# Optimization experiments

Hardware: AMD Instinct MI355X
Metric: run time of the kernel (lower is better)

Reference implementation:

```python
import jax, jax.numpy as jnp
import numpy as np

BLK = 128            # weight_block_size for w8a16 blockwise dequant
H = 1024             # hidden_size
I = 512              # moe_intermediate_size
E = 64               # n_routed_experts
T = 512              # tokens (seq_len)
K = 6                # num_experts_per_tok
G = 8                # n_group
TG = 3               # topk_group
NSH = 2              # n_shared_experts
I2 = I * NSH         # shared expert intermediate size
ROUTED_SCALE = 2.5
NORM_TOPK = True


def dq(w_int8, scale, blk=BLK):
    """Blockwise w8a16 dequant: w [..., M, N] int8, scale [..., M/blk, N/blk] f32."""
    *lead, M, N = w_int8.shape
    w = w_int8.astype(scale.dtype).reshape(*lead, M // blk, blk, N // blk, blk)
    return (w * scale[..., :, None, :, None]).reshape(*lead, M, N)


def setup_inputs() -> dict:
    key = jax.random.key(0)
    ks = jax.random.split(key, 16)
    ri = lambda k, shp: jax.random.randint(k, shp, -8, 8, dtype=jnp.int8)
    rs = lambda k, shp: jax.random.uniform(k, shp, minval=0.01, maxval=0.03, dtype=jnp.float32)
    return {
        "x": jax.random.normal(ks[0], (T, H), jnp.float32),
        "gate_w": jax.random.normal(ks[1], (E, H), jnp.float32) * 0.02,  # router gate [E,H]
        "wg": ri(ks[2], (E, I, H)),  "sg": rs(ks[3], (E, I // BLK, H // BLK)),
        "wu": ri(ks[4], (E, I, H)),  "su": rs(ks[5], (E, I // BLK, H // BLK)),
        "wd": ri(ks[6], (E, I, H)),  "sd": rs(ks[7], (E, I // BLK, H // BLK)),  # down, transposed layout [I,H]
        "sh_wg": ri(ks[8], (I2, H)),  "sh_sg": rs(ks[9], (I2 // BLK, H // BLK)),
        "sh_wu": ri(ks[10], (I2, H)), "sh_su": rs(ks[11], (I2 // BLK, H // BLK)),
        "sh_wd": ri(ks[12], (I2, H)), "sh_sd": rs(ks[13], (I2 // BLK, H // BLK)),
    }


def _moe(x, gate_w, wg, sg, wu, su, wd, sd, sh_wg, sh_sg, sh_wu, sh_su, sh_wd, sh_sd):
    Tn = x.shape[0]
    # --- router: sigmoid scoring + group-limited top-k ---
    scores = jax.nn.sigmoid(x @ gate_w.T)                       # [T, E]
    gsz = E // G
    group_scores = scores.reshape(Tn, G, gsz).max(axis=-1)      # [T, G]
    _, gidx = jax.lax.top_k(group_scores, TG)                   # [T, TG]
    gmask = jax.nn.one_hot(gidx, G, dtype=scores.dtype).sum(1)  # [T, G]
    emask = jnp.repeat(gmask, gsz, axis=-1)                     # [T, E]
    masked = jnp.where(emask > 0, scores, -jnp.inf)
    w, idx = jax.lax.top_k(masked, K)                           # [T, K]
    if NORM_TOPK:
        w = w / (w.sum(-1, keepdims=True) + 1e-20)
    w = w * ROUTED_SCALE
    # per-token combine weights over experts
    comb = (jax.nn.one_hot(idx, E, dtype=x.dtype) * w[:, :, None]).sum(1)  # [T, E]

    # --- routed experts: dequantized silu-gated MLPs, masked dense combine ---
    Wg, Wu, Wd = dq(wg, sg), dq(wu, su), dq(wd, sd)             # [E, I, H]
    g = jnp.einsum('th,eih->eti', x, Wg)                        # [E, T, I]
    u = jnp.einsum('th,eih->eti', x, Wu)
    hmid = jax.nn.silu(g) * u
    y = jnp.einsum('eti,eih->eth', hmid, Wd)                    # [E, T, H]
    routed = jnp.einsum('eth,te->th', y, comb)                  # [T, H]

    # --- shared experts MLP ---
    Sg, Su, Sd = dq(sh_wg, sh_sg), dq(sh_wu, sh_su), dq(sh_wd, sh_sd)
    shared = (jax.nn.silu(x @ Sg.T) * (x @ Su.T)) @ Sd          # [T, H]
    return routed + shared


def reference(x, gate_w, wg, sg, wu, su, wd, sd, sh_wg, sh_sg, sh_wu, sh_su, sh_wd, sh_sd):
    return _moe(x, gate_w, wg, sg, wu, su, wd, sd,
                sh_wg, sh_sg, sh_wu, sh_su, sh_wd, sh_sd)
```

## Files before the change

### kernel.cpp

```cpp
#include <hip/hip_runtime.h>
#include <math.h>
#include <stdint.h>

#define T_   512
#define H_   1024
#define I_   512
#define E_   64
#define K_   6
#define G_   8
#define TG_  3
#define EB_  80

typedef _Float16 h8 __attribute__((ext_vector_type(8)));
typedef _Float16 h4v __attribute__((ext_vector_type(4)));
typedef float    f4 __attribute__((ext_vector_type(4)));

__global__ __launch_bounds__(64) void router_k(
    const float* __restrict__ x, const float* __restrict__ gw,
    int* __restrict__ cnt, int* __restrict__ tlist, float* __restrict__ wlist)
{
  const int t   = blockIdx.x;
  const int tid = threadIdx.x;
  __shared__ float sx[H_];
  __shared__ float sc[E_];

  for (int h4 = tid; h4 < H_/4; h4 += 64)
    ((float4*)sx)[h4] = ((const float4*)(x + (size_t)t*H_))[h4];
  __syncthreads();

  const float* wr = gw + (size_t)tid * H_;
  float acc = 0.f;
  for (int h = 0; h < H_; h += 4) {
    float4 xv = *(const float4*)(sx + h);
    float4 wv = *(const float4*)(wr + h);
    acc = fmaf(xv.x, wv.x, acc); acc = fmaf(xv.y, wv.y, acc);
    acc = fmaf(xv.z, wv.z, acc); acc = fmaf(xv.w, wv.w, acc);
  }
  sc[tid] = 1.f / (1.f + expf(-acc));
  __syncthreads();

  if (tid == 0) {
    float gs[G_];
    #pragma unroll
    for (int g = 0; g < G_; g++) {
      float m = sc[g*8];
      #pragma unroll
      for (int j = 1; j < 8; j++) m = fmaxf(m, sc[g*8+j]);
      gs[g] = m;
    }
    unsigned gp = 0;
    for (int r = 0; r < TG_; r++) {
      int best = 0; float bv = -1e30f;
      for (int g = 0; g < G_; g++)
        if (!((gp >> g) & 1) && gs[g] > bv) { bv = gs[g]; best = g; }
      gp |= 1u << best;
    }
    int   eidx[K_]; float ew[K_];
    unsigned long long em = 0ull;
    float wsum = 0.f;
    for (int r = 0; r < K_; r++) {
      int best = 0; float bv = -1e30f;
      for (int e = 0; e < E_; e++) {
        if (!((gp >> (e >> 3)) & 1)) continue;
        if ((em >> e) & 1ull) continue;
        if (sc[e] > bv) { bv = sc[e]; best = e; }
      }
      em |= 1ull << best; eidx[r] = best; ew[r] = bv; wsum += bv;
    }
    const float inv = 2.5f / (wsum + 1e-20f);
    for (int r = 0; r < K_; r++) {
      int e = eidx[r];
      int pos = atomicAdd(&cnt[e], 1);
      tlist[e*T_ + pos] = (t << 13) | (t*K_ + r);
      wlist[e*T_ + pos] = ew[r] * inv;
    }
  }
}

__global__ void pseudo_init_k(int* cnt, int* tlist, float* wlist) {
  int s = blockIdx.x*256 + threadIdx.x;
  if (s == 0) { cnt[64] = T_; cnt[65] = T_; }
  if (s < 1024) {
    int e = 64 + (s >> 9);
    int t = s & 511;
    tlist[e*T_ + t] = (t << 13) | (3072 + s);
    wlist[e*T_ + t] = 1.0f;
  }
}

__global__ __launch_bounds__(256) void xh_prep_k(
    const float* __restrict__ x, _Float16* __restrict__ xh)
{
  int i = blockIdx.x*256 + threadIdx.x;
  float4 v = ((const float4*)x)[i];
  h4v o = { (_Float16)v.x, (_Float16)v.y, (_Float16)v.z, (_Float16)v.w };
  *(h4v*)(xh + (size_t)i*4) = o;
}

__device__ __forceinline__ void eb_decode(int eb, const int* cnt,
                                          int& e, int& lo, int& hi) {
  if (eb < E_) { e = eb; lo = 0; hi = cnt[e]; }
  else { int q = (eb - E_) & 7; e = E_ + ((eb - E_) >> 3); lo = q*64; hi = lo + 64; }
}

__device__ __forceinline__ h8 cvt8i(int4 a, int4 b) {
  union { _Float16 f[8]; h8 v; } t;
  t.f[0]=(_Float16)a.x; t.f[1]=(_Float16)a.y; t.f[2]=(_Float16)a.z; t.f[3]=(_Float16)a.w;
  t.f[4]=(_Float16)b.x; t.f[5]=(_Float16)b.y; t.f[6]=(_Float16)b.z; t.f[7]=(_Float16)b.w;
  return t.v;
}

#define NKT_G 16

#define GU_STEP(KT, WN)                                                       \
  do {                                                                        \
    asm volatile("s_waitcnt vmcnt(" #WN ") lgkmcnt(0)" ::: "memory");         \
    __builtin_amdgcn_sched_barrier(0);                                        \
    __builtin_amdgcn_s_barrier();                                             \
    if ((KT) + 1 < NKT_G)                                                     \
      *(h8*)(wdst + (((KT)+1)&1)*4608) =                                      \
          cvt8i(Wr[((KT)+1)%3][0], Wr[((KT)+1)%3][1]);                        \
    if ((KT) + 3 < NKT_G) {                                                   \
      Wr[((KT)+3)%3][0] = *(const int4*)(wsrc + ((KT)+3)*64);                 \
      Wr[((KT)+3)%3][1] = *(const int4*)(wsrc + ((KT)+3)*64 + 4);             \
    }                                                                         \
    {                                                                         \
      const char* tb = tb0 + (((KT)&1))*4608;                                 \
      h8 bg0 = *(const h8*)(tb);                                              \
      h8 bg1 = *(const h8*)(tb + 64);                                         \
      h8 bu0 = *(const h8*)(tb + 2304);                                       \
      h8 bu1 = *(const h8*)(tb + 2304 + 64);                                  \
      if (((KT)&1) == 0) { partg = (f4){0.f,0.f,0.f,0.f}; partu = partg; }    \
      partg = __builtin_amdgcn_mfma_f32_16x16x32_f16(Ar[(KT)%3][0], bg0, partg, 0,0,0); \
      partg = __builtin_amdgcn_mfma_f32_16x16x32_f16(Ar[(KT)%3][1], bg1, partg, 0,0,0); \
      partu = __builtin_amdgcn_mfma_f32_16x16x32_f16(Ar[(KT)%3][0], bu0, partu, 0,0,0); \
      partu = __builtin_amdgcn_mfma_f32_16x16x32_f16(Ar[(KT)%3][1], bu1, partu, 0,0,0); \
      if (((KT)&1) == 1) {                                                    \
        totg += partg * sgv[(KT)>>1];                                         \
        totu += partu * suv[(KT)>>1];                                         \
      }                                                                       \
    }                                                                         \
    if ((KT) + 3 < NKT_G) {                                                   \
      Ar[((KT)+3)%3][0] = *(const h8*)(ax + ((KT)+3)*64);                     \
      Ar[((KT)+3)%3][1] = *(const h8*)(ax + ((KT)+3)*64 + 32);                \
    }                                                                         \
  } while (0)

__global__ __launch_bounds__(256, 6) void gateup_k(
    const _Float16* __restrict__ xh,
    const int* __restrict__ wg, const float* __restrict__ sg,
    const int* __restrict__ wu, const float* __restrict__ su,
    const int* __restrict__ shwg, const float* __restrict__ shsg,
    const int* __restrict__ shwu, const float* __restrict__ shsu,
    const int* __restrict__ cnt, const int* __restrict__ tlist,
    const float* __restrict__ wlist,
    _Float16* __restrict__ hmid)
{
  const int ic = blockIdx.x;
  const int eb = blockIdx.y;
  int e, lo, hi;
  eb_decode(eb, cnt, e, lo, hi);
  if (hi <= lo) return;

  const int tid  = threadIdx.x;
  const int lane = tid & 63;
  const int wv   = tid >> 6;
  const int mr   = lane & 15;
  const int quad = lane >> 4;

  const int *wgb, *wub; const float *sgp, *sup; int sib;
  if (e < E_) {
    wgb = wg + (size_t)e*I_*H_;  wub = wu + (size_t)e*I_*H_;
    sgp = sg + e*32;  sup = su + e*32;  sib = ic >> 3;
  } else {
    int hf = e - E_;
    wgb = shwg + (size_t)hf*512*H_;  wub = shwu + (size_t)hf*512*H_;
    sgp = shsg;  sup = shsu;  sib = hf*4 + (ic >> 3);
  }
  float sgv[8], suv[8];
  #pragma unroll
  for (int b = 0; b < 8; b++) { sgv[b] = sgp[sib*8+b]; suv[b] = sup[sib*8+b]; }

  __shared__ _Float16 tile[2][2][16][72];
  __shared__ int stok[64]; __shared__ int srw[64]; __shared__ float swt[64];
  char* tilebytes = (char*)&tile[0][0][0][0];

  const int smat = wv >> 1;
  const int srow = (wv & 1)*8 + (lane >> 3);
  const int* wsrc = (smat ? wub : wgb) + (size_t)(ic*16 + srow)*H_ + (lane & 7)*8;
  char* wdst = tilebytes + smat*2304 + srow*144 + (lane & 7)*16;
  const char* tb0 = tilebytes + mr*144 + quad*16;

  int4 Wr[3][2];
  h8   Ar[3][2];

  for (int base = lo; base < hi; base += 64) {
    __syncthreads();
    if (tid < 64) {
      int slot = base + tid;
      if (slot < hi) {
        int ent = tlist[e*T_ + slot];
        stok[tid] = ent >> 13; srw[tid] = ent & 8191; swt[tid] = wlist[e*T_ + slot];
      } else { stok[tid] = -1; srw[tid] = 0; swt[tid] = 0.f; }
    }
    __syncthreads();

    int tk = stok[wv*16 + mr]; if (tk < 0) tk = 0;
    const _Float16* ax = xh + (size_t)tk*H_ + quad*8;

    f4 totg = (f4){0.f,0.f,0.f,0.f}, totu = totg, partg = totg, partu = totg;

    Wr[0][0] = *(const int4*)(wsrc);       Wr[0][1] = *(const int4*)(wsrc + 4);
    Ar[0][0] = *(const h8*)(ax);           Ar[0][1] = *(const h8*)(ax + 32);
    Wr[1][0] = *(const int4*)(wsrc + 64);  Wr[1][1] = *(const int4*)(wsrc + 68);
    Ar[1][0] = *(const h8*)(ax + 64);      Ar[1][1] = *(const h8*)(ax + 96);
    Wr[2][0] = *(const int4*)(wsrc + 128); Wr[2][1] = *(const int4*)(wsrc + 132);
    Ar[2][0] = *(const h8*)(ax + 128);     Ar[2][1] = *(const h8*)(ax + 160);
    *(h8*)(wdst) = cvt8i(Wr[0][0], Wr[0][1]);

    GU_STEP(0,6);  GU_STEP(1,6);  GU_STEP(2,6);  GU_STEP(3,6);
    GU_STEP(4,6);  GU_STEP(5,6);  GU_STEP(6,6);  GU_STEP(7,6);
    GU_STEP(8,6);  GU_STEP(9,6);  GU_STEP(10,6); GU_STEP(11,6);
    GU_STEP(12,6); GU_STEP(13,6); GU_STEP(14,2); GU_STEP(15,0);

    const int icol = ic*16 + mr;
    #pragma unroll
    for (int r = 0; r < 4; r++) {
      int sl = wv*16 + quad*4 + r;
      if (stok[sl] >= 0) {
        float g = totg[r];
        float m = g / (1.f + expf(-g)) * totu[r] * swt[sl];
        hmid[(size_t)srw[sl]*I_ + icol] = (_Float16)m;
      }
    }
  }
}
#undef GU_STEP

#define NKT_D 8

#define DN_LDW(S, KT)                                                         \
  do {                                                                        \
    Wr[S][0] = *(const int2*)(dsrc + (size_t)((KT)*64 + 0)*H_);               \
    Wr[S][1] = *(const int2*)(dsrc + (size_t)((KT)*64 + 1)*H_);               \
    Wr[S][2] = *(const int2*)(dsrc + (size_t)((KT)*64 + 2)*H_);               \
    Wr[S][3] = *(const int2*)(dsrc + (size_t)((KT)*64 + 3)*H_);               \
  } while (0)

#define DN_WRITE(S, BUF)                                                      \
  do {                                                                        \
    union { _Float16 f[4]; h4v v; } v0, v1;                                   \
    v0.f[0]=(_Float16)Wr[S][0].x; v0.f[1]=(_Float16)Wr[S][1].x;               \
    v0.f[2]=(_Float16)Wr[S][2].x; v0.f[3]=(_Float16)Wr[S][3].x;               \
    v1.f[0]=(_Float16)Wr[S][0].y; v1.f[1]=(_Float16)Wr[S][1].y;               \
    v1.f[2]=(_Float16)Wr[S][2].y; v1.f[3]=(_Float16)Wr[S][3].y;               \
    *(h4v*)(ddst + (BUF)*4608)       = v0.v;                                  \
    *(h4v*)(ddst + (BUF)*4608 + 144) = v1.v;                                  \
  } while (0)

#define DN_STEP(KT, WN)                                                       \
  do {                                                                        \
    asm volatile("s_waitcnt vmcnt(" #WN ") lgkmcnt(0)" ::: "memory");         \
    __builtin_amdgcn_sched_barrier(0);                                        \
    __builtin_amdgcn_s_barrier();                                             \
    if ((KT) + 1 < NKT_D) DN_WRITE(((KT)+1)%3, ((KT)+1)&1);                   \
    if ((KT) + 3 < NKT_D) DN_LDW(((KT)+3)%3, (KT)+3);                         \
    {                                                                         \
      const char* tb = tb0 + (((KT)&1))*4608;                                 \
      h8 b00 = *(const h8*)(tb);                                              \
      h8 b01 = *(const h8*)(tb + 64);                                         \
      h8 b10 = *(const h8*)(tb + 2304);                                       \
      h8 b11 = *(const h8*)(tb + 2304 + 64);                                  \
      if (((KT)&1) == 0) { part0 = (f4){0.f,0.f,0.f,0.f}; part1 = part0; }    \
      part0 = __builtin_amdgcn_mfma_f32_16x16x32_f16(Ar[(KT)%3][0], b00, part0, 0,0,0); \
      part0 = __builtin_amdgcn_mfma_f32_16x16x32_f16(Ar[(KT)%3][1], b01, part0, 0,0,0); \
      part1 = __builtin_amdgcn_mfma_f32_16x16x32_f16(Ar[(KT)%3][0], b10, part1, 0,0,0); \
      part1 = __builtin_amdgcn_mfma_f32_16x16x32_f16(Ar[(KT)%3][1], b11, part1, 0,0,0); \
      if (((KT)&1) == 1) {                                                    \
        tot0 += part0 * sdv[(KT)>>1];                                         \
        tot1 += part1 * sdv[(KT)>>1];                                         \
      }                                                                       \
    }                                                                         \
    if ((KT) + 3 < NKT_D) {                                                   \
      Ar[((KT)+3)%3][0] = *(const h8*)(ap + ((KT)+3)*64);                     \
      Ar[((KT)+3)%3][1] = *(const h8*)(ap + ((KT)+3)*64 + 32);                \
    }                                                                         \
  } while (0)

__global__ __launch_bounds__(256, 6) void down_k(
    const int* __restrict__ wd, const float* __restrict__ sd,
    const int* __restrict__ shwd, const float* __restrict__ shsd,
    const int* __restrict__ cnt, const int* __restrict__ tlist,
    const _Float16* __restrict__ hmid, float* __restrict__ scr)
{
  const int hc = blockIdx.x;
  const int eb = blockIdx.y;
  int e, lo, hi;
  eb_decode(eb, cnt, e, lo, hi);
  if (hi <= lo) return;

  const int tid  = threadIdx.x;
  const int lane = tid & 63;
  const int wv   = tid >> 6;
  const int mr   = lane & 15;
  const int quad = lane >> 4;

  const int* wb; const float* sdp; int sib0;
  if (e < E_) { wb = wd + (size_t)e*I_*H_;        sdp = sd + e*32;  sib0 = 0; }
  else { int hf = e - E_; wb = shwd + (size_t)hf*512*H_; sdp = shsd; sib0 = hf*4; }
  float sdv[4];
  #pragma unroll
  for (int ib = 0; ib < 4; ib++) sdv[ib] = sdp[(sib0+ib)*8 + (hc >> 2)];

  __shared__ _Float16 tile[2][32][72];
  __shared__ int stok[64]; __shared__ int srw[64];
  char* tilebytes = (char*)&tile[0][0][0];

  const int rg = lane >> 4;
  const int* dsrc = wb + (size_t)(wv*16 + rg*4)*H_ + hc*32 + (lane & 15)*2;
  char* ddst = tilebytes + ((lane & 15)*2)*144 + (wv*16 + rg*4)*2;
  const char* tb0 = tilebytes + mr*144 + quad*16;

  int2 Wr[3][4];
  h8   Ar[3][2];

  for (int base = lo; base < hi; base += 64) {
    __syncthreads();
    if (tid < 64) {
      int slot = base + tid;
      if (slot < hi) {
        int ent = tlist[e*T_ + slot];
        stok[tid] = ent >> 13; srw[tid] = ent & 8191;
      } else { stok[tid] = -1; srw[tid] = 0; }
    }
    __syncthreads();

    const _Float16* ap = hmid + (size_t)srw[wv*16 + mr]*I_ + quad*8;

    f4 tot0 = (f4){0.f,0.f,0.f,0.f}, tot1 = tot0, part0 = tot0, part1 = tot0;

    DN_LDW(0, 0);
    Ar[0][0] = *(const h8*)(ap);        Ar[0][1] = *(const h8*)(ap + 32);
    DN_LDW(1, 1);
    Ar[1][0] = *(const h8*)(ap + 64);   Ar[1][1] = *(const h8*)(ap + 96);
    DN_LDW(2, 2);
    Ar[2][0] = *(const h8*)(ap + 128);  Ar[2][1] = *(const h8*)(ap + 160);
    DN_WRITE(0, 0);

    DN_STEP(0,6); DN_STEP(1,6); DN_STEP(2,6); DN_STEP(3,6);
    DN_STEP(4,6); DN_STEP(5,6); DN_STEP(6,2); DN_STEP(7,0);

    #pragma unroll
    for (int r = 0; r < 4; r++) {
      int sl = wv*16 + quad*4 + r;
      if (stok[sl] >= 0) {
        int t  = stok[sl];
        int sr = srw[sl];
        int rank = (sr < 3072) ? (sr - t*6) : (6 + ((sr - 3072) >> 9));
        float* dst = scr + (size_t)(t*8 + rank)*H_ + hc*32 + mr;
        dst[0]  = tot0[r];
        dst[16] = tot1[r];
      }
    }
  }
}
#undef DN_STEP
#undef DN_WRITE
#undef DN_LDW

__global__ __launch_bounds__(256) void combine_k(
    const float* __restrict__ scr, float* __restrict__ out)
{
  int i = blockIdx.x*256 + threadIdx.x;
  int t = i >> 8;
  int c = i & 255;
  const float4* base = (const float4*)(scr + (size_t)t*8*H_) + c;
  float4 s = base[0];
  #pragma unroll
  for (int r = 1; r < 8; r++) {
    float4 v = base[(size_t)r*(H_/4)];
    s.x += v.x; s.y += v.y; s.z += v.z; s.w += v.w;
  }
  ((float4*)out)[i] = s;
}

extern "C" void kernel_launch(void* const* d_in, const int* in_sizes, int n_in,
                              void* d_out, int out_size, void* d_ws, size_t ws_size,
                              hipStream_t stream) {
  (void)in_sizes; (void)n_in; (void)ws_size; (void)out_size;
  const float* x    = (const float*)d_in[0];
  const float* gw   = (const float*)d_in[1];
  const int*   wg   = (const int*  )d_in[2];
  const float* sg   = (const float*)d_in[3];
  const int*   wu   = (const int*  )d_in[4];
  const float* su   = (const float*)d_in[5];
  const int*   wd   = (const int*  )d_in[6];
  const float* sd   = (const float*)d_in[7];
  const int*   shwg = (const int*  )d_in[8];
  const float* shsg = (const float*)d_in[9];
  const int*   shwu = (const int*  )d_in[10];
  const float* shsu = (const float*)d_in[11];
  const int*   shwd = (const int*  )d_in[12];
  const float* shsd = (const float*)d_in[13];
  float* out = (float*)d_out;

  char* ws = (char*)d_ws;
  int*      cnt   = (int*     ) ws;
  int*      tlist = (int*     )(ws + 1024);
  float*    wlist = (float*   )(ws + 1024 + 66*T_*4);
  _Float16* hmid  = (_Float16*)(ws + 1024 + 2*66*T_*4);
  _Float16* xh    = (_Float16*)(ws + 1024 + 2*66*T_*4 + 4096*I_*2);
  float*    scr   = (float*   )(ws + 1024 + 2*66*T_*4 + 4096*I_*2 + T_*H_*2);

  hipMemsetAsync(cnt, 0, 1024, stream);
  xh_prep_k<<<T_*H_/1024, 256, 0, stream>>>(x, xh);
  router_k<<<T_, 64, 0, stream>>>(x, gw, cnt, tlist, wlist);
  pseudo_init_k<<<4, 256, 0, stream>>>(cnt, tlist, wlist);
  gateup_k<<<dim3(32, EB_), 256, 0, stream>>>(xh, wg, sg, wu, su,
                                              shwg, shsg, shwu, shsu,
                                              cnt, tlist, wlist, hmid);
  down_k<<<dim3(32, EB_), 256, 0, stream>>>(wd, sd, shwd, shsd,
                                            cnt, tlist, hmid, scr);
  combine_k<<<T_*H_/1024, 256, 0, stream>>>(scr, out);
}
```

Measured before the change: 593.4 us.

## Widen MoE output tiles and fold blockwise scales into dequantized weights

Gate/up now computes a 64-column tile per block with 512 threads (8 waves split 4×2 over rows and columns) instead of 16 columns. Down now covers 64 output columns per block instead of 32, so each token row loaded from hmid is reused across more columns. The per-block int8 scales are multiplied into the weights during the int8→fp16 conversion, which removes the partial-accumulator and scale-multiply steps and lets the K loop use finer 32-wide steps with deeper unrolling. The cost is more registers and LDS per block and fewer blocks in the grid, and rounding the scaled weights to fp16 changes precision slightly.

```diff
diff --git a/kernel.cpp b/kernel.cpp
--- a/kernel.cpp
+++ b/kernel.cpp
@@ -103,50 +103,46 @@
   else { int q = (eb - E_) & 7; e = E_ + ((eb - E_) >> 3); lo = q*64; hi = lo + 64; }
 }
 
-__device__ __forceinline__ h8 cvt8i(int4 a, int4 b) {
+__device__ __forceinline__ h8 cvt8(int4 a, int4 b, float s) {
   union { _Float16 f[8]; h8 v; } t;
-  t.f[0]=(_Float16)a.x; t.f[1]=(_Float16)a.y; t.f[2]=(_Float16)a.z; t.f[3]=(_Float16)a.w;
-  t.f[4]=(_Float16)b.x; t.f[5]=(_Float16)b.y; t.f[6]=(_Float16)b.z; t.f[7]=(_Float16)b.w;
+  t.f[0]=(_Float16)((float)a.x*s); t.f[1]=(_Float16)((float)a.y*s);
+  t.f[2]=(_Float16)((float)a.z*s); t.f[3]=(_Float16)((float)a.w*s);
+  t.f[4]=(_Float16)((float)b.x*s); t.f[5]=(_Float16)((float)b.y*s);
+  t.f[6]=(_Float16)((float)b.z*s); t.f[7]=(_Float16)((float)b.w*s);
   return t.v;
 }
 
-#define NKT_G 16
+#define NKT_G 32
 
 #define GU_STEP(KT, WN)                                                       \
   do {                                                                        \
     asm volatile("s_waitcnt vmcnt(" #WN ") lgkmcnt(0)" ::: "memory");         \
     __builtin_amdgcn_sched_barrier(0);                                        \
     __builtin_amdgcn_s_barrier();                                             \
+    __builtin_amdgcn_sched_barrier(0);                                        \
     if ((KT) + 1 < NKT_G)                                                     \
-      *(h8*)(wdst + (((KT)+1)&1)*4608) =                                      \
-          cvt8i(Wr[((KT)+1)%3][0], Wr[((KT)+1)%3][1]);                        \
+      *(h8*)(wdst + (((KT)+1)&1)*5120) =                                      \
+          cvt8(Wr[((KT)+1)%3][0], Wr[((KT)+1)%3][1], sv[((KT)+1)>>2]);        \
     if ((KT) + 3 < NKT_G) {                                                   \
-      Wr[((KT)+3)%3][0] = *(const int4*)(wsrc + ((KT)+3)*64);                 \
-      Wr[((KT)+3)%3][1] = *(const int4*)(wsrc + ((KT)+3)*64 + 4);             \
+      Wr[((KT)+3)%3][0] = *(const int4*)(wsrc + ((KT)+3)*32);                 \
+      Wr[((KT)+3)%3][1] = *(const int4*)(wsrc + ((KT)+3)*32 + 4);             \
     }                                                                         \
     {                                                                         \
-      const char* tb = tb0 + (((KT)&1))*4608;                                 \
-      h8 bg0 = *(const h8*)(tb);                                              \
-      h8 bg1 = *(const h8*)(tb + 64);                                         \
-      h8 bu0 = *(const h8*)(tb + 2304);                                       \
-      h8 bu1 = *(const h8*)(tb + 2304 + 64);                                  \
-      if (((KT)&1) == 0) { partg = (f4){0.f,0.f,0.f,0.f}; partu = partg; }    \
-      partg = __builtin_amdgcn_mfma_f32_16x16x32_f16(Ar[(KT)%3][0], bg0, partg, 0,0,0); \
-      partg = __builtin_amdgcn_mfma_f32_16x16x32_f16(Ar[(KT)%3][1], bg1, partg, 0,0,0); \
-      partu = __builtin_amdgcn_mfma_f32_16x16x32_f16(Ar[(KT)%3][0], bu0, partu, 0,0,0); \
-      partu = __builtin_amdgcn_mfma_f32_16x16x32_f16(Ar[(KT)%3][1], bu1, partu, 0,0,0); \
-      if (((KT)&1) == 1) {                                                    \
-        totg += partg * sgv[(KT)>>1];                                         \
-        totu += partu * suv[(KT)>>1];                                         \
-      }                                                                       \
+      const _Float16* tb = lds0 + ((KT)&1)*5120;                              \
+      h8 bg0 = *(const h8*)(tb + ro0);                                        \
+      h8 bg1 = *(const h8*)(tb + ro1);                                        \
+      h8 bu0 = *(const h8*)(tb + 2560 + ro0);                                 \
+      h8 bu1 = *(const h8*)(tb + 2560 + ro1);                                 \
+      accg0 = __builtin_amdgcn_mfma_f32_16x16x32_f16(Ar[(KT)%4], bg0, accg0, 0,0,0); \
+      accg1 = __builtin_amdgcn_mfma_f32_16x16x32_f16(Ar[(KT)%4], bg1, accg1, 0,0,0); \
+      accu0 = __builtin_amdgcn_mfma_f32_16x16x32_f16(Ar[(KT)%4], bu0, accu0, 0,0,0); \
+      accu1 = __builtin_amdgcn_mfma_f32_16x16x32_f16(Ar[(KT)%4], bu1, accu1, 0,0,0); \
     }                                                                         \
-    if ((KT) + 3 < NKT_G) {                                                   \
-      Ar[((KT)+3)%3][0] = *(const h8*)(ax + ((KT)+3)*64);                     \
-      Ar[((KT)+3)%3][1] = *(const h8*)(ax + ((KT)+3)*64 + 32);                \
-    }                                                                         \
+    if ((KT) + 3 < NKT_G)                                                     \
+      Ar[((KT)+3)%4] = *(const h8*)(ax + ((KT)+3)*32);                        \
   } while (0)
 
-__global__ __launch_bounds__(256, 6) void gateup_k(
+__global__ __launch_bounds__(512, 6) void gateup_k(
     const _Float16* __restrict__ xh,
     const int* __restrict__ wg, const float* __restrict__ sg,
     const int* __restrict__ wu, const float* __restrict__ su,
@@ -167,32 +163,37 @@
   const int wv   = tid >> 6;
   const int mr   = lane & 15;
   const int quad = lane >> 4;
+  const int wm   = wv & 3;
+  const int wn   = wv >> 2;
 
   const int *wgb, *wub; const float *sgp, *sup; int sib;
   if (e < E_) {
     wgb = wg + (size_t)e*I_*H_;  wub = wu + (size_t)e*I_*H_;
-    sgp = sg + e*32;  sup = su + e*32;  sib = ic >> 3;
+    sgp = sg + e*32;  sup = su + e*32;  sib = ic >> 1;
   } else {
     int hf = e - E_;
     wgb = shwg + (size_t)hf*512*H_;  wub = shwu + (size_t)hf*512*H_;
-    sgp = shsg;  sup = shsu;  sib = hf*4 + (ic >> 3);
-  }
-  float sgv[8], suv[8];
+    sgp = shsg;  sup = shsu;  sib = hf*4 + (ic >> 1);
+  }
+
+  const int smat = tid >> 8;
+  const int sr   = (tid >> 2) & 63;
+  const int sseg = tid & 3;
+  const int* wsrc = (smat ? wub : wgb) + (size_t)(ic*64 + sr)*H_ + sseg*8;
+  const float* ssc = (smat ? sup : sgp) + sib*8;
+  float sv[8];
   #pragma unroll
-  for (int b = 0; b < 8; b++) { sgv[b] = sgp[sib*8+b]; suv[b] = sup[sib*8+b]; }
-
-  __shared__ _Float16 tile[2][2][16][72];
+  for (int b = 0; b < 8; b++) sv[b] = ssc[b];
+
+  __shared__ _Float16 wlds[2*2*64*40];
   __shared__ int stok[64]; __shared__ int srw[64]; __shared__ float swt[64];
-  char* tilebytes = (char*)&tile[0][0][0][0];
-
-  const int smat = wv >> 1;
-  const int srow = (wv & 1)*8 + (lane >> 3);
-  const int* wsrc = (smat ? wub : wgb) + (size_t)(ic*16 + srow)*H_ + (lane & 7)*8;
-  char* wdst = tilebytes + smat*2304 + srow*144 + (lane & 7)*16;
-  const char* tb0 = tilebytes + mr*144 + quad*16;
+  _Float16* lds0 = wlds;
+  _Float16* wdst = wlds + smat*2560 + sr*40 + sseg*8;
+  const int ro0 = (wn*32 + mr)*40 + quad*8;
+  const int ro1 = ro0 + 16*40;
 
   int4 Wr[3][2];
-  h8   Ar[3][2];
+  h8   Ar[4];
 
   for (int base = lo; base < hi; base += 64) {
     __syncthreads();
@@ -205,57 +206,68 @@
     }
     __syncthreads();
 
-    int tk = stok[wv*16 + mr]; if (tk < 0) tk = 0;
+    int tk = stok[wm*16 + mr]; if (tk < 0) tk = 0;
     const _Float16* ax = xh + (size_t)tk*H_ + quad*8;
 
-    f4 totg = (f4){0.f,0.f,0.f,0.f}, totu = totg, partg = totg, partu = totg;
-
-    Wr[0][0] = *(const int4*)(wsrc);       Wr[0][1] = *(const int4*)(wsrc + 4);
-    Ar[0][0] = *(const h8*)(ax);           Ar[0][1] = *(const h8*)(ax + 32);
-    Wr[1][0] = *(const int4*)(wsrc + 64);  Wr[1][1] = *(const int4*)(wsrc + 68);
-    Ar[1][0] = *(const h8*)(ax + 64);      Ar[1][1] = *(const h8*)(ax + 96);
-    Wr[2][0] = *(const int4*)(wsrc + 128); Wr[2][1] = *(const int4*)(wsrc + 132);
-    Ar[2][0] = *(const h8*)(ax + 128);     Ar[2][1] = *(const h8*)(ax + 160);
-    *(h8*)(wdst) = cvt8i(Wr[0][0], Wr[0][1]);
-
-    GU_STEP(0,6);  GU_STEP(1,6);  GU_STEP(2,6);  GU_STEP(3,6);
-    GU_STEP(4,6);  GU_STEP(5,6);  GU_STEP(6,6);  GU_STEP(7,6);
-    GU_STEP(8,6);  GU_STEP(9,6);  GU_STEP(10,6); GU_STEP(11,6);
-    GU_STEP(12,6); GU_STEP(13,6); GU_STEP(14,2); GU_STEP(15,0);
-
-    const int icol = ic*16 + mr;
+    f4 accg0 = (f4){0.f,0.f,0.f,0.f}, accg1 = accg0, accu0 = accg0, accu1 = accg0;
+
+    Wr[0][0] = *(const int4*)(wsrc);      Wr[0][1] = *(const int4*)(wsrc + 4);
+    Ar[0]    = *(const h8*)(ax);
+    Wr[1][0] = *(const int4*)(wsrc + 32); Wr[1][1] = *(const int4*)(wsrc + 36);
+    Ar[1]    = *(const h8*)(ax + 32);
+    Wr[2][0] = *(const int4*)(wsrc + 64); Wr[2][1] = *(const int4*)(wsrc + 68);
+    Ar[2]    = *(const h8*)(ax + 64);
+    asm volatile("s_waitcnt vmcnt(7)" ::: "memory");
+    __builtin_amdgcn_sched_barrier(0);
+    *(h8*)(wdst) = cvt8(Wr[0][0], Wr[0][1], sv[0]);
+
+    GU_STEP(0,4);  GU_STEP(1,4);  GU_STEP(2,4);  GU_STEP(3,4);
+    GU_STEP(4,4);  GU_STEP(5,4);  GU_STEP(6,4);  GU_STEP(7,4);
+    GU_STEP(8,4);  GU_STEP(9,4);  GU_STEP(10,4); GU_STEP(11,4);
+    GU_STEP(12,4); GU_STEP(13,4); GU_STEP(14,4); GU_STEP(15,4);
+    GU_STEP(16,4); GU_STEP(17,4); GU_STEP(18,4); GU_STEP(19,4);
+    GU_STEP(20,4); GU_STEP(21,4); GU_STEP(22,4); GU_STEP(23,4);
+    GU_STEP(24,4); GU_STEP(25,4); GU_STEP(26,4); GU_STEP(27,4);
+    GU_STEP(28,4); GU_STEP(29,4); GU_STEP(30,1); GU_STEP(31,0);
+
+    const int icol = ic*64 + wn*32 + mr;
     #pragma unroll
     for (int r = 0; r < 4; r++) {
-      int sl = wv*16 + quad*4 + r;
+      int sl = wm*16 + quad*4 + r;
       if (stok[sl] >= 0) {
-        float g = totg[r];
-        float m = g / (1.f + expf(-g)) * totu[r] * swt[sl];
-        hmid[(size_t)srw[sl]*I_ + icol] = (_Float16)m;
+        float wt = swt[sl];
+        float g0 = accg0[r];
+        float m0 = g0 / (1.f + expf(-g0)) * accu0[r] * wt;
+        float g1 = accg1[r];
+        float m1 = g1 / (1.f + expf(-g1)) * accu1[r] * wt;
+        _Float16* hp = hmid + (size_t)srw[sl]*I_ + icol;
+        hp[0]  = (_Float16)m0;
+        hp[16] = (_Float16)m1;
       }
     }
   }
 }
 #undef GU_STEP
 
-#define NKT_D 8
+#define NKT_D 16
 
 #define DN_LDW(S, KT)                                                         \
   do {                                                                        \
-    Wr[S][0] = *(const int2*)(dsrc + (size_t)((KT)*64 + 0)*H_);               \
-    Wr[S][1] = *(const int2*)(dsrc + (size_t)((KT)*64 + 1)*H_);               \
-    Wr[S][2] = *(const int2*)(dsrc + (size_t)((KT)*64 + 2)*H_);               \
-    Wr[S][3] = *(const int2*)(dsrc + (size_t)((KT)*64 + 3)*H_);               \
+    Wr[S][0] = *(const int2*)(dsrc + (size_t)((KT)*32 + 0)*H_);               \
+    Wr[S][1] = *(const int2*)(dsrc + (size_t)((KT)*32 + 1)*H_);               \
+    Wr[S][2] = *(const int2*)(dsrc + (size_t)((KT)*32 + 2)*H_);               \
+    Wr[S][3] = *(const int2*)(dsrc + (size_t)((KT)*32 + 3)*H_);               \
   } while (0)
 
-#define DN_WRITE(S, BUF)                                                      \
+#define DN_WRITE(S, BUF, SC)                                                  \
   do {                                                                        \
     union { _Float16 f[4]; h4v v; } v0, v1;                                   \
-    v0.f[0]=(_Float16)Wr[S][0].x; v0.f[1]=(_Float16)Wr[S][1].x;               \
-    v0.f[2]=(_Float16)Wr[S][2].x; v0.f[3]=(_Float16)Wr[S][3].x;               \
-    v1.f[0]=(_Float16)Wr[S][0].y; v1.f[1]=(_Float16)Wr[S][1].y;               \
-    v1.f[2]=(_Float16)Wr[S][2].y; v1.f[3]=(_Float16)Wr[S][3].y;               \
-    *(h4v*)(ddst + (BUF)*4608)       = v0.v;                                  \
-    *(h4v*)(ddst + (BUF)*4608 + 144) = v1.v;                                  \
+    v0.f[0]=(_Float16)((float)Wr[S][0].x*(SC)); v0.f[1]=(_Float16)((float)Wr[S][1].x*(SC)); \
+    v0.f[2]=(_Float16)((float)Wr[S][2].x*(SC)); v0.f[3]=(_Float16)((float)Wr[S][3].x*(SC)); \
+    v1.f[0]=(_Float16)((float)Wr[S][0].y*(SC)); v1.f[1]=(_Float16)((float)Wr[S][1].y*(SC)); \
+    v1.f[2]=(_Float16)((float)Wr[S][2].y*(SC)); v1.f[3]=(_Float16)((float)Wr[S][3].y*(SC)); \
+    *(h4v*)(ddst0 + (BUF)*2560)      = v0.v;                                  \
+    *(h4v*)(ddst0 + (BUF)*2560 + 40) = v1.v;                                  \
   } while (0)
 
 #define DN_STEP(KT, WN)                                                       \
@@ -263,28 +275,22 @@
     asm volatile("s_waitcnt vmcnt(" #WN ") lgkmcnt(0)" ::: "memory");         \
     __builtin_amdgcn_sched_barrier(0);                                        \
     __builtin_amdgcn_s_barrier();                                             \
-    if ((KT) + 1 < NKT_D) DN_WRITE(((KT)+1)%3, ((KT)+1)&1);                   \
+    __builtin_amdgcn_sched_barrier(0);                                        \
+    if ((KT) + 1 < NKT_D) DN_WRITE(((KT)+1)%3, ((KT)+1)&1, scd[((KT)+1)>>2]); \
     if ((KT) + 3 < NKT_D) DN_LDW(((KT)+3)%3, (KT)+3);                         \
     {                                                                         \
-      const char* tb = tb0 + (((KT)&1))*4608;                                 \
-      h8 b00 = *(const h8*)(tb);                                              \
-      h8 b01 = *(const h8*)(tb + 64);                                         \
-      h8 b10 = *(const h8*)(tb + 2304);                                       \
-      h8 b11 = *(const h8*)(tb + 2304 + 64);                                  \
-      if (((KT)&1) == 0) { part0 = (f4){0.f,0.f,0.f,0.f}; part1 = part0; }    \
-      part0 = __builtin_amdgcn_mfma_f32_16x16x32_f16(Ar[(KT)%3][0], b00, part0, 0,0,0); \
-      part0 = __builtin_amdgcn_mfma_f32_16x16x32_f16(Ar[(KT)%3][1], b01, part0, 0,0,0); \
-      part1 = __builtin_amdgcn_mfma_f32_16x16x32_f16(Ar[(KT)%3][0], b10, part1, 0,0,0); \
-      part1 = __builtin_amdgcn_mfma_f32_16x16x32_f16(Ar[(KT)%3][1], b11, part1, 0,0,0); \
-      if (((KT)&1) == 1) {                                                    \
-        tot0 += part0 * sdv[(KT)>>1];                                         \
-        tot1 += part1 * sdv[(KT)>>1];                                         \
-      }                                                                       \
+      const _Float16* tb = lds0 + ((KT)&1)*2560;                              \
+      h8 b0 = *(const h8*)(tb + ro0);                                         \
+      h8 b1 = *(const h8*)(tb + ro1);                                         \
+      h8 b2 = *(const h8*)(tb + ro2);                                         \
+      h8 b3 = *(const h8*)(tb + ro3);                                         \
+      tot0 = __builtin_amdgcn_mfma_f32_16x16x32_f16(Ar[(KT)%4], b0, tot0, 0,0,0); \
+      tot1 = __builtin_amdgcn_mfma_f32_16x16x32_f16(Ar[(KT)%4], b1, tot1, 0,0,0); \
+      tot2 = __builtin_amdgcn_mfma_f32_16x16x32_f16(Ar[(KT)%4], b2, tot2, 0,0,0); \
+      tot3 = __builtin_amdgcn_mfma_f32_16x16x32_f16(Ar[(KT)%4], b3, tot3, 0,0,0); \
     }                                                                         \
-    if ((KT) + 3 < NKT_D) {                                                   \
-      Ar[((KT)+3)%3][0] = *(const h8*)(ap + ((KT)+3)*64);                     \
-      Ar[((KT)+3)%3][1] = *(const h8*)(ap + ((KT)+3)*64 + 32);                \
-    }                                                                         \
+    if ((KT) + 3 < NKT_D)                                                     \
+      Ar[((KT)+3)%4] = *(const h8*)(ap + ((KT)+3)*32);                        \
   } while (0)
 
 __global__ __launch_bounds__(256, 6) void down_k(
@@ -308,21 +314,25 @@
   const int* wb; const float* sdp; int sib0;
   if (e < E_) { wb = wd + (size_t)e*I_*H_;        sdp = sd + e*32;  sib0 = 0; }
   else { int hf = e - E_; wb = shwd + (size_t)hf*512*H_; sdp = shsd; sib0 = hf*4; }
-  float sdv[4];
+  float scd[4];
   #pragma unroll
-  for (int ib = 0; ib < 4; ib++) sdv[ib] = sdp[(sib0+ib)*8 + (hc >> 2)];
-
-  __shared__ _Float16 tile[2][32][72];
+  for (int ib = 0; ib < 4; ib++) scd[ib] = sdp[(sib0+ib)*8 + (hc >> 1)];
+
+  const int ig = tid >> 5;
+  const int hp = tid & 31;
+  const int* dsrc = wb + (size_t)(ig*4)*H_ + hc*64 + hp*2;
+
+  __shared__ _Float16 wlds[2*64*40];
   __shared__ int stok[64]; __shared__ int srw[64];
-  char* tilebytes = (char*)&tile[0][0][0];
-
-  const int rg = lane >> 4;
-  const int* dsrc = wb + (size_t)(wv*16 + rg*4)*H_ + hc*32 + (lane & 15)*2;
-  char* ddst = tilebytes + ((lane & 15)*2)*144 + (wv*16 + rg*4)*2;
-  const char* tb0 = tilebytes + mr*144 + quad*16;
+  _Float16* lds0  = wlds;
+  _Float16* ddst0 = wlds + (hp*2)*40 + ig*4;
+  const int ro0 = (     mr)*40 + quad*8;
+  const int ro1 = (16 + mr)*40 + quad*8;
+  const int ro2 = (32 + mr)*40 + quad*8;
+  const int ro3 = (48 + mr)*40 + quad*8;
 
   int2 Wr[3][4];
-  h8   Ar[3][2];
+  h8   Ar[4];
 
   for (int base = lo; base < hi; base += 64) {
     __syncthreads();
@@ -337,18 +347,19 @@
 
     const _Float16* ap = hmid + (size_t)srw[wv*16 + mr]*I_ + quad*8;
 
-    f4 tot0 = (f4){0.f,0.f,0.f,0.f}, tot1 = tot0, part0 = tot0, part1 = tot0;
-
-    DN_LDW(0, 0);
-    Ar[0][0] = *(const h8*)(ap);        Ar[0][1] = *(const h8*)(ap + 32);
-    DN_LDW(1, 1);
-    Ar[1][0] = *(const h8*)(ap + 64);   Ar[1][1] = *(const h8*)(ap + 96);
-    DN_LDW(2, 2);
-    Ar[2][0] = *(const h8*)(ap + 128);  Ar[2][1] = *(const h8*)(ap + 160);
-    DN_WRITE(0, 0);
-
-    DN_STEP(0,6); DN_STEP(1,6); DN_STEP(2,6); DN_STEP(3,6);
-    DN_STEP(4,6); DN_STEP(5,6); DN_STEP(6,2); DN_STEP(7,0);
+    f4 tot0 = (f4){0.f,0.f,0.f,0.f}, tot1 = tot0, tot2 = tot0, tot3 = tot0;
+
+    DN_LDW(0, 0); Ar[0] = *(const h8*)(ap);
+    DN_LDW(1, 1); Ar[1] = *(const h8*)(ap + 32);
+    DN_LDW(2, 2); Ar[2] = *(const h8*)(ap + 64);
+    asm volatile("s_waitcnt vmcnt(10)" ::: "memory");
+    __builtin_amdgcn_sched_barrier(0);
+    DN_WRITE(0, 0, scd[0]);
+
+    DN_STEP(0,6);  DN_STEP(1,6);  DN_STEP(2,6);  DN_STEP(3,6);
+    DN_STEP(4,6);  DN_STEP(5,6);  DN_STEP(6,6);  DN_STEP(7,6);
+    DN_STEP(8,6);  DN_STEP(9,6);  DN_STEP(10,6); DN_STEP(11,6);
+    DN_STEP(12,6); DN_STEP(13,6); DN_STEP(14,1); DN_STEP(15,0);
 
     #pragma unroll
     for (int r = 0; r < 4; r++) {
@@ -357,9 +368,11 @@
         int t  = stok[sl];
         int sr = srw[sl];
         int rank = (sr < 3072) ? (sr - t*6) : (6 + ((sr - 3072) >> 9));
-        float* dst = scr + (size_t)(t*8 + rank)*H_ + hc*32 + mr;
+        float* dst = scr + (size_t)(t*8 + rank)*H_ + hc*64 + mr;
         dst[0]  = tot0[r];
         dst[16] = tot1[r];
+        dst[32] = tot2[r];
+        dst[48] = tot3[r];
       }
     }
   }
@@ -416,10 +429,10 @@
   xh_prep_k<<<T_*H_/1024, 256, 0, stream>>>(x, xh);
   router_k<<<T_, 64, 0, stream>>>(x, gw, cnt, tlist, wlist);
   pseudo_init_k<<<4, 256, 0, stream>>>(cnt, tlist, wlist);
-  gateup_k<<<dim3(32, EB_), 256, 0, stream>>>(xh, wg, sg, wu, su,
-                                              shwg, shsg, shwu, shsu,
-                                              cnt, tlist, wlist, hmid);
-  down_k<<<dim3(32, EB_), 256, 0, stream>>>(wd, sd, shwd, shsd,
+  gateup_k<<<dim3(8, EB_), 512, 0, stream>>>(xh, wg, sg, wu, su,
+                                             shwg, shsg, shwu, shsu,
+                                             cnt, tlist, wlist, hmid);
+  down_k<<<dim3(16, EB_), 256, 0, stream>>>(wd, sd, shwd, shsd,
                                             cnt, tlist, hmid, scr);
   combine_k<<<T_*H_/1024, 256, 0, stream>>>(scr, out);
 }
```

Result: faster. 557.3 us (-6.1%).
